# Optimization experiments

Measured on AMD Instinct MI355X. Metric: run time of the kernel, lower is better.

## Reference

```python
import jax, jax.numpy as jnp
import numpy as np
import math

B, N = 64, 16384
POS_IN, HID, DIR_IN = 63, 128, 27
COLOR_IN = HID + DIR_IN  # 155
POS_W, POS_B = POS_IN * HID, HID          # 8064, 128
SIG_W, SIG_B = HID * 1, 1                  # 128, 1
COL_W, COL_B = COLOR_IN * 3, 3             # 465... actually 155*3=465? no: 465
TOTAL = POS_W + POS_B + SIG_W + SIG_B + COL_W + COL_B  # 8717


def pos_encode(x, num_freqs):
    # x: [..., 3] -> [..., 3 + 2*3*num_freqs], order: x, (sin f0, cos f0, sin f1, cos f1, ...)
    freqs = (2.0 ** jnp.arange(num_freqs, dtype=x.dtype)) * math.pi  # [L]
    xb = x[..., None, :] * freqs[:, None]                            # [..., L, 3]
    sc = jnp.stack([jnp.sin(xb), jnp.cos(xb)], axis=-2)              # [..., L, 2, 3]
    sc = sc.reshape(*x.shape[:-1], num_freqs * 2 * x.shape[-1])
    return jnp.concatenate([x, sc], axis=-1)


def setup_inputs() -> dict:
    key = jax.random.key(0)
    k1, k2, k3 = jax.random.split(key, 3)
    positions = jax.random.normal(k1, (B, N, 3), dtype=jnp.float32)
    directions = jax.random.normal(k2, (B, N, 3), dtype=jnp.float32)
    params = jax.random.normal(k3, (B, TOTAL), dtype=jnp.float32) * 0.1
    return {"positions": positions, "directions": directions, "params": params}


def reference(positions, directions, params):
    pos_enc = pos_encode(positions, 10)   # [B, N, 63]
    dir_enc = pos_encode(directions, 4)   # [B, N, 27]

    i = 0
    pw = params[:, i:i + POS_W].reshape(B, HID, POS_IN); i += POS_W
    pb = params[:, i:i + POS_B]; i += POS_B
    sw = params[:, i:i + SIG_W].reshape(B, 1, HID); i += SIG_W
    sb = params[:, i:i + SIG_B]; i += SIG_B
    cw = params[:, i:i + COL_W].reshape(B, 3, COLOR_IN); i += COL_W
    cb = params[:, i:i + COL_B]

    h = jnp.einsum('bnd,bhd->bnh', pos_enc, pw) + pb[:, None, :]
    h = jax.nn.relu(h)                                   # [B, N, 128]
    sigma = jnp.einsum('bnh,boh->bno', h, sw) + sb[:, None, :]  # [B, N, 1]
    h_dir = jnp.concatenate([h, dir_enc], axis=-1)       # [B, N, 155]
    rgb = jnp.einsum('bnc,boc->bno', h_dir, cw) + cb[:, None, :]
    rgb = jax.nn.sigmoid(rgb)                            # [B, N, 3]
    return sigma, rgb
```

## Files before the change

kernel.cpp:

```cpp
#include <hip/hip_runtime.h>
#include <hip/hip_bf16.h>


#define NB 64
#define NRAY 16384
#define NTOTAL 8789
#define PI_F 3.14159265358979323846f

typedef short bf16x8 __attribute__((ext_vector_type(8)));
typedef float f32x16 __attribute__((ext_vector_type(16)));

union U8 { unsigned u[4]; bf16x8 v; };

__device__ __forceinline__ unsigned bfbits(float x) {
    __hip_bfloat16 h = __float2bfloat16(x);
    return (unsigned)*reinterpret_cast<unsigned short*>(&h);
}
__device__ __forceinline__ unsigned pk2(float a, float b) {
    return bfbits(a) | (bfbits(b) << 16);
}

__global__ __launch_bounds__(256, 2) void nerf_mfma_kernel(
    const float* __restrict__ pos,
    const float* __restrict__ dir,
    const float* __restrict__ params,
    float* __restrict__ out)
{
    const int tid  = threadIdx.x;
    const int lane = tid & 63;
    const int wid  = tid >> 6;
    const int hi   = lane >> 5;
    const int l31  = lane & 31;

    const int b     = blockIdx.x >> 4;
    const int chunk = (blockIdx.x & 15) << 10;
    const float* __restrict__ p = params + b * NTOTAL;

    __shared__ uint4 encs[2048];
    char* encb = reinterpret_cast<char*>(encs);

    bf16x8 aw[4][4];
    #pragma unroll
    for (int mt = 0; mt < 4; ++mt) {
        const int hrow = mt * 32 + l31;
        const float* wrow = p + hrow * 63;
        const float bias = p[8064 + hrow];
        #pragma unroll
        for (int ks = 0; ks < 4; ++ks) {
            U8 u;
            #pragma unroll
            for (int j = 0; j < 4; ++j) {
                const int k0 = ks * 16 + hi * 8 + 2 * j;
                const int k1 = k0 + 1;
                const float e0 = (k0 < 3) ? wrow[k0] : (k0 == 3 ? bias : wrow[k0 - 1]);
                const float e1 = (k1 < 3) ? wrow[k1] : (k1 == 3 ? bias : wrow[k1 - 1]);
                u.u[j] = pk2(e0, e1);
            }
            aw[mt][ks] = u.v;
        }
    }
    bf16x8 haw[8];
    {
        const int r = l31 & 3;
        const float* w2 = (r == 0) ? (p + 8192) : (p + 8321 + (r - 1) * 155);
        #pragma unroll
        for (int s = 0; s < 8; ++s) {
            const int base = 32 * (s >> 1) + 16 * (s & 1) + 4 * hi;
            U8 u;
            #pragma unroll
            for (int j = 0; j < 4; ++j) {
                const int i0 = 2 * j, i1 = 2 * j + 1;
                u.u[j] = pk2(w2[base + (i0 & 3) + 8 * (i0 >> 2)],
                             w2[base + (i1 & 3) + 8 * (i1 >> 2)]);
            }
            haw[s] = u.v;
        }
    }

    f32x16 FZ;
    #pragma unroll
    for (int i = 0; i < 16; ++i) FZ[i] = 0.f;

    const float sb  = p[8320];
    const float cb0 = p[8786], cb1 = p[8787], cb2 = p[8788];
    const float* __restrict__ cwr = p + 8321 + 128;
    const float* __restrict__ cwg = p + 8321 + 155 + 128;
    const float* __restrict__ cwb2 = p + 8321 + 310 + 128;

    const int rayBlock = b * NRAY + chunk;
    float* __restrict__ rgbout = out + (long)NB * NRAY;
    const long pbase = (long)(rayBlock + tid) * 3;

    float3 P  = *reinterpret_cast<const float3*>(pos + pbase);
    float3 Dv = *reinterpret_cast<const float3*>(dir + pbase);

    #pragma unroll 1
    for (int it = 0; it < 4; ++it) {
        const int ray = rayBlock + it * 256 + tid;

        float3 Pn, Dn;
        if (it < 3) {
            Pn = *reinterpret_cast<const float3*>(pos + pbase + (it + 1) * 768);
            Dn = *reinterpret_cast<const float3*>(dir + pbase + (it + 1) * 768);
        }

        {
            asm volatile("s_waitcnt lgkmcnt(0)" ::: "memory");
            const int swz = (tid & 7) << 4;
            char* myrow = encb + tid * 128;
            float s0, c0, s1, c1, s2, c2;
            __sincosf(P.x * PI_F, &s0, &c0);
            __sincosf(P.y * PI_F, &s1, &c1);
            __sincosf(P.z * PI_F, &s2, &c2);
            unsigned wb[4];
            wb[0] = pk2(P.x, P.y);
            wb[1] = pk2(P.z, 1.0f);
            #pragma unroll
            for (int f = 0; f < 10; ++f) {
                const int w = 2 + 3 * f;
                wb[(w + 0) & 3] = pk2(s0, s1);
                if (((w + 0) & 3) == 3) {
                    uint4 v; v.x = wb[0]; v.y = wb[1]; v.z = wb[2]; v.w = wb[3];
                    *reinterpret_cast<uint4*>(myrow + ((((w + 0) >> 2) * 16) ^ swz)) = v;
                }
                wb[(w + 1) & 3] = pk2(s2, c0);
                if (((w + 1) & 3) == 3) {
                    uint4 v; v.x = wb[0]; v.y = wb[1]; v.z = wb[2]; v.w = wb[3];
                    *reinterpret_cast<uint4*>(myrow + ((((w + 1) >> 2) * 16) ^ swz)) = v;
                }
                wb[(w + 2) & 3] = pk2(c1, c2);
                if (((w + 2) & 3) == 3) {
                    uint4 v; v.x = wb[0]; v.y = wb[1]; v.z = wb[2]; v.w = wb[3];
                    *reinterpret_cast<uint4*>(myrow + ((((w + 2) >> 2) * 16) ^ swz)) = v;
                }
                if (f < 9) {
                    float t;
                    t = 2.f * s0 * c0; c0 = fmaf(-2.f * s0, s0, 1.f); s0 = t;
                    t = 2.f * s1 * c1; c1 = fmaf(-2.f * s1, s1, 1.f); s1 = t;
                    t = 2.f * s2 * c2; c2 = fmaf(-2.f * s2, s2, 1.f); s2 = t;
                }
            }
            asm volatile("s_waitcnt lgkmcnt(0)" ::: "memory");
        }

        float hres[2][4];
        #pragma unroll
        for (int nt = 0; nt < 2; ++nt) {
            const int row = wid * 64 + nt * 32 + l31;
            const int swz = (row & 7) << 4;
            bf16x8 be[4];
            #pragma unroll
            for (int ks = 0; ks < 4; ++ks)
                be[ks] = *reinterpret_cast<const bf16x8*>(
                    encb + row * 128 + (((ks * 32 + hi * 16)) ^ swz));

            f32x16 haccA, haccB;
            #pragma unroll
            for (int mt = 0; mt < 4; ++mt) {
                f32x16 accm = __builtin_amdgcn_mfma_f32_32x32x16_bf16(aw[mt][0], be[0], FZ, 0, 0, 0);
                accm = __builtin_amdgcn_mfma_f32_32x32x16_bf16(aw[mt][1], be[1], accm, 0, 0, 0);
                accm = __builtin_amdgcn_mfma_f32_32x32x16_bf16(aw[mt][2], be[2], accm, 0, 0, 0);
                accm = __builtin_amdgcn_mfma_f32_32x32x16_bf16(aw[mt][3], be[3], accm, 0, 0, 0);

                #pragma unroll
                for (int t = 0; t < 2; ++t) {
                    const int rb = t * 8;
                    U8 u;
                    #pragma unroll
                    for (int j = 0; j < 4; ++j)
                        u.u[j] = pk2(fmaxf(accm[rb + 2 * j], 0.f),
                                     fmaxf(accm[rb + 2 * j + 1], 0.f));
                    const int s = 2 * mt + t;
                    if (t == 0)
                        haccA = __builtin_amdgcn_mfma_f32_32x32x16_bf16(
                            haw[s], u.v, (mt == 0) ? FZ : haccA, 0, 0, 0);
                    else
                        haccB = __builtin_amdgcn_mfma_f32_32x32x16_bf16(
                            haw[s], u.v, (mt == 0) ? FZ : haccB, 0, 0, 0);
                }
            }
            hres[nt][0] = haccA[0] + haccB[0];
            hres[nt][1] = haccA[1] + haccB[1];
            hres[nt][2] = haccA[2] + haccB[2];
            hres[nt][3] = haccA[3] + haccB[3];
        }

        const float hv0 = hi ? hres[1][0] : hres[0][0];
        const float hv1 = hi ? hres[1][1] : hres[0][1];
        const float hv2 = hi ? hres[1][2] : hres[0][2];
        const float hv3 = hi ? hres[1][3] : hres[0][3];

        float sig = hv0 + sb;
        float cr  = hv1 + cb0;
        float cg  = hv2 + cb1;
        float cbl = hv3 + cb2;

        {
            float s0, c0, s1, c1, s2, c2;
            __sincosf(Dv.x * PI_F, &s0, &c0);
            __sincosf(Dv.y * PI_F, &s1, &c1);
            __sincosf(Dv.z * PI_F, &s2, &c2);
            cr  = fmaf(Dv.x, cwr[0], cr);  cg  = fmaf(Dv.x, cwg[0], cg);  cbl = fmaf(Dv.x, cwb2[0], cbl);
            cr  = fmaf(Dv.y, cwr[1], cr);  cg  = fmaf(Dv.y, cwg[1], cg);  cbl = fmaf(Dv.y, cwb2[1], cbl);
            cr  = fmaf(Dv.z, cwr[2], cr);  cg  = fmaf(Dv.z, cwg[2], cg);  cbl = fmaf(Dv.z, cwb2[2], cbl);
            #pragma unroll
            for (int f = 0; f < 4; ++f) {
                const int j = 3 + 6 * f;
                cr = fmaf(s0, cwr[j+0], cr); cg = fmaf(s0, cwg[j+0], cg); cbl = fmaf(s0, cwb2[j+0], cbl);
                cr = fmaf(s1, cwr[j+1], cr); cg = fmaf(s1, cwg[j+1], cg); cbl = fmaf(s1, cwb2[j+1], cbl);
                cr = fmaf(s2, cwr[j+2], cr); cg = fmaf(s2, cwg[j+2], cg); cbl = fmaf(s2, cwb2[j+2], cbl);
                cr = fmaf(c0, cwr[j+3], cr); cg = fmaf(c0, cwg[j+3], cg); cbl = fmaf(c0, cwb2[j+3], cbl);
                cr = fmaf(c1, cwr[j+4], cr); cg = fmaf(c1, cwg[j+4], cg); cbl = fmaf(c1, cwb2[j+4], cbl);
                cr = fmaf(c2, cwr[j+5], cr); cg = fmaf(c2, cwg[j+5], cg); cbl = fmaf(c2, cwb2[j+5], cbl);
                if (f < 3) {
                    float t;
                    t = 2.f * s0 * c0; c0 = fmaf(-2.f * s0, s0, 1.f); s0 = t;
                    t = 2.f * s1 * c1; c1 = fmaf(-2.f * s1, s1, 1.f); s1 = t;
                    t = 2.f * s2 * c2; c2 = fmaf(-2.f * s2, s2, 1.f); s2 = t;
                }
            }
        }

        cr  = 1.0f / (1.0f + __expf(-cr));
        cg  = 1.0f / (1.0f + __expf(-cg));
        cbl = 1.0f / (1.0f + __expf(-cbl));

        out[ray] = sig;
        float3 rgbv; rgbv.x = cr; rgbv.y = cg; rgbv.z = cbl;
        *reinterpret_cast<float3*>(rgbout + (long)ray * 3) = rgbv;

        P = Pn; Dv = Dn;
    }
}

extern "C" void kernel_launch(void* const* d_in, const int* in_sizes, int n_in,
                              void* d_out, int out_size, void* d_ws, size_t ws_size,
                              hipStream_t stream) {
    const float* pos    = (const float*)d_in[0];
    const float* dirs   = (const float*)d_in[1];
    const float* params = (const float*)d_in[2];
    float* out = (float*)d_out;

    dim3 grid(1024);
    dim3 block(256);
    nerf_mfma_kernel<<<grid, block, 0, stream>>>(pos, dirs, params, out);
}
```

Before: 53.72 us.

## Software-pipeline positional encoding of next ray tile behind MFMA work

```diff
diff --git a/kernel.cpp b/kernel.cpp
--- a/kernel.cpp
+++ b/kernel.cpp
@@ -12,12 +12,10 @@
 
 union U8 { unsigned u[4]; bf16x8 v; };
 
-__device__ __forceinline__ unsigned bfbits(float x) {
-    __hip_bfloat16 h = __float2bfloat16(x);
-    return (unsigned)*reinterpret_cast<unsigned short*>(&h);
-}
 __device__ __forceinline__ unsigned pk2(float a, float b) {
-    return bfbits(a) | (bfbits(b) << 16);
+    float2 t; t.x = a; t.y = b;
+    __hip_bfloat162 h = __float22bfloat162_rn(t);
+    return *reinterpret_cast<unsigned*>(&h);
 }
 
 __global__ __launch_bounds__(256, 2) void nerf_mfma_kernel(
@@ -83,84 +81,82 @@
 
     const float sb  = p[8320];
     const float cb0 = p[8786], cb1 = p[8787], cb2 = p[8788];
-    const float* __restrict__ cwr = p + 8321 + 128;
-    const float* __restrict__ cwg = p + 8321 + 155 + 128;
+    const float* __restrict__ cwr  = p + 8321 + 128;
+    const float* __restrict__ cwg  = p + 8321 + 155 + 128;
     const float* __restrict__ cwb2 = p + 8321 + 310 + 128;
 
     const int rayBlock = b * NRAY + chunk;
     float* __restrict__ rgbout = out + (long)NB * NRAY;
-    const long pbase = (long)(rayBlock + tid) * 3;
-
-    float3 P  = *reinterpret_cast<const float3*>(pos + pbase);
-    float3 Dv = *reinterpret_cast<const float3*>(dir + pbase);
+    const long pb0 = (long)(rayBlock + tid) * 3;
+
+    auto encode_row = [&](const float3 Pv) {
+        const int swz = (tid & 7) << 4;
+        char* myrow = encb + tid * 128;
+        float s0, c0, s1, c1, s2, c2;
+        __sincosf(Pv.x * PI_F, &s0, &c0);
+        __sincosf(Pv.y * PI_F, &s1, &c1);
+        __sincosf(Pv.z * PI_F, &s2, &c2);
+        unsigned w[32];
+        w[0] = pk2(Pv.x, Pv.y);
+        w[1] = pk2(Pv.z, 1.0f);
+        #pragma unroll
+        for (int f = 0; f < 10; ++f) {
+            w[2 + 3 * f] = pk2(s0, s1);
+            w[3 + 3 * f] = pk2(s2, c0);
+            w[4 + 3 * f] = pk2(c1, c2);
+            if (f < 9) {
+                float t;
+                t = 2.f * s0 * c0; c0 = fmaf(-2.f * s0, s0, 1.f); s0 = t;
+                t = 2.f * s1 * c1; c1 = fmaf(-2.f * s1, s1, 1.f); s1 = t;
+                t = 2.f * s2 * c2; c2 = fmaf(-2.f * s2, s2, 1.f); s2 = t;
+            }
+        }
+        #pragma unroll
+        for (int cq = 0; cq < 8; ++cq) {
+            uint4 v;
+            v.x = w[4 * cq + 0]; v.y = w[4 * cq + 1];
+            v.z = w[4 * cq + 2]; v.w = w[4 * cq + 3];
+            *reinterpret_cast<uint4*>(myrow + ((cq * 16) ^ swz)) = v;
+        }
+    };
+
+    float3 P0 = *reinterpret_cast<const float3*>(pos + pb0);
+    float3 Pn = *reinterpret_cast<const float3*>(pos + pb0 + 768);
+    float3 Dc = *reinterpret_cast<const float3*>(dir + pb0);
+    encode_row(P0);
 
     #pragma unroll 1
     for (int it = 0; it < 4; ++it) {
         const int ray = rayBlock + it * 256 + tid;
 
-        float3 Pn, Dn;
-        if (it < 3) {
-            Pn = *reinterpret_cast<const float3*>(pos + pbase + (it + 1) * 768);
-            Dn = *reinterpret_cast<const float3*>(dir + pbase + (it + 1) * 768);
-        }
-
-        {
-            asm volatile("s_waitcnt lgkmcnt(0)" ::: "memory");
-            const int swz = (tid & 7) << 4;
-            char* myrow = encb + tid * 128;
-            float s0, c0, s1, c1, s2, c2;
-            __sincosf(P.x * PI_F, &s0, &c0);
-            __sincosf(P.y * PI_F, &s1, &c1);
-            __sincosf(P.z * PI_F, &s2, &c2);
-            unsigned wb[4];
-            wb[0] = pk2(P.x, P.y);
-            wb[1] = pk2(P.z, 1.0f);
-            #pragma unroll
-            for (int f = 0; f < 10; ++f) {
-                const int w = 2 + 3 * f;
-                wb[(w + 0) & 3] = pk2(s0, s1);
-                if (((w + 0) & 3) == 3) {
-                    uint4 v; v.x = wb[0]; v.y = wb[1]; v.z = wb[2]; v.w = wb[3];
-                    *reinterpret_cast<uint4*>(myrow + ((((w + 0) >> 2) * 16) ^ swz)) = v;
-                }
-                wb[(w + 1) & 3] = pk2(s2, c0);
-                if (((w + 1) & 3) == 3) {
-                    uint4 v; v.x = wb[0]; v.y = wb[1]; v.z = wb[2]; v.w = wb[3];
-                    *reinterpret_cast<uint4*>(myrow + ((((w + 1) >> 2) * 16) ^ swz)) = v;
-                }
-                wb[(w + 2) & 3] = pk2(c1, c2);
-                if (((w + 2) & 3) == 3) {
-                    uint4 v; v.x = wb[0]; v.y = wb[1]; v.z = wb[2]; v.w = wb[3];
-                    *reinterpret_cast<uint4*>(myrow + ((((w + 2) >> 2) * 16) ^ swz)) = v;
-                }
-                if (f < 9) {
-                    float t;
-                    t = 2.f * s0 * c0; c0 = fmaf(-2.f * s0, s0, 1.f); s0 = t;
-                    t = 2.f * s1 * c1; c1 = fmaf(-2.f * s1, s1, 1.f); s1 = t;
-                    t = 2.f * s2 * c2; c2 = fmaf(-2.f * s2, s2, 1.f); s2 = t;
-                }
-            }
-            asm volatile("s_waitcnt lgkmcnt(0)" ::: "memory");
-        }
-
-        float hres[2][4];
+        float3 Pn2, Dn;
+        if (it < 2) Pn2 = *reinterpret_cast<const float3*>(pos + pb0 + (it + 2) * 768);
+        if (it < 3) Dn  = *reinterpret_cast<const float3*>(dir + pb0 + (it + 1) * 768);
+
+        bf16x8 be[2][4];
         #pragma unroll
         for (int nt = 0; nt < 2; ++nt) {
             const int row = wid * 64 + nt * 32 + l31;
             const int swz = (row & 7) << 4;
-            bf16x8 be[4];
             #pragma unroll
             for (int ks = 0; ks < 4; ++ks)
-                be[ks] = *reinterpret_cast<const bf16x8*>(
-                    encb + row * 128 + (((ks * 32 + hi * 16)) ^ swz));
-
-            f32x16 haccA, haccB;
+                be[nt][ks] = *reinterpret_cast<const bf16x8*>(
+                    encb + row * 128 + ((ks * 32 + hi * 16) ^ swz));
+        }
+
+        if (it < 3) encode_row(Pn);
+
+        __builtin_amdgcn_s_setprio(1);
+        float hres[2][4];
+        #pragma unroll
+        for (int nt = 0; nt < 2; ++nt) {
+            f32x16 hacc;
             #pragma unroll
             for (int mt = 0; mt < 4; ++mt) {
-                f32x16 accm = __builtin_amdgcn_mfma_f32_32x32x16_bf16(aw[mt][0], be[0], FZ, 0, 0, 0);
-                accm = __builtin_amdgcn_mfma_f32_32x32x16_bf16(aw[mt][1], be[1], accm, 0, 0, 0);
-                accm = __builtin_amdgcn_mfma_f32_32x32x16_bf16(aw[mt][2], be[2], accm, 0, 0, 0);
-                accm = __builtin_amdgcn_mfma_f32_32x32x16_bf16(aw[mt][3], be[3], accm, 0, 0, 0);
+                f32x16 accm = __builtin_amdgcn_mfma_f32_32x32x16_bf16(aw[mt][0], be[nt][0], FZ, 0, 0, 0);
+                accm = __builtin_amdgcn_mfma_f32_32x32x16_bf16(aw[mt][1], be[nt][1], accm, 0, 0, 0);
+                accm = __builtin_amdgcn_mfma_f32_32x32x16_bf16(aw[mt][2], be[nt][2], accm, 0, 0, 0);
+                accm = __builtin_amdgcn_mfma_f32_32x32x16_bf16(aw[mt][3], be[nt][3], accm, 0, 0, 0);
 
                 #pragma unroll
                 for (int t = 0; t < 2; ++t) {
@@ -170,20 +166,14 @@
                     for (int j = 0; j < 4; ++j)
                         u.u[j] = pk2(fmaxf(accm[rb + 2 * j], 0.f),
                                      fmaxf(accm[rb + 2 * j + 1], 0.f));
-                    const int s = 2 * mt + t;
-                    if (t == 0)
-                        haccA = __builtin_amdgcn_mfma_f32_32x32x16_bf16(
-                            haw[s], u.v, (mt == 0) ? FZ : haccA, 0, 0, 0);
-                    else
-                        haccB = __builtin_amdgcn_mfma_f32_32x32x16_bf16(
-                            haw[s], u.v, (mt == 0) ? FZ : haccB, 0, 0, 0);
+                    hacc = __builtin_amdgcn_mfma_f32_32x32x16_bf16(
+                        haw[2 * mt + t], u.v, (mt == 0 && t == 0) ? FZ : hacc, 0, 0, 0);
                 }
             }
-            hres[nt][0] = haccA[0] + haccB[0];
-            hres[nt][1] = haccA[1] + haccB[1];
-            hres[nt][2] = haccA[2] + haccB[2];
-            hres[nt][3] = haccA[3] + haccB[3];
-        }
+            hres[nt][0] = hacc[0]; hres[nt][1] = hacc[1];
+            hres[nt][2] = hacc[2]; hres[nt][3] = hacc[3];
+        }
+        __builtin_amdgcn_s_setprio(0);
 
         const float hv0 = hi ? hres[1][0] : hres[0][0];
         const float hv1 = hi ? hres[1][1] : hres[0][1];
@@ -197,12 +187,12 @@
 
         {
             float s0, c0, s1, c1, s2, c2;
-            __sincosf(Dv.x * PI_F, &s0, &c0);
-            __sincosf(Dv.y * PI_F, &s1, &c1);
-            __sincosf(Dv.z * PI_F, &s2, &c2);
-            cr  = fmaf(Dv.x, cwr[0], cr);  cg  = fmaf(Dv.x, cwg[0], cg);  cbl = fmaf(Dv.x, cwb2[0], cbl);
-            cr  = fmaf(Dv.y, cwr[1], cr);  cg  = fmaf(Dv.y, cwg[1], cg);  cbl = fmaf(Dv.y, cwb2[1], cbl);
-            cr  = fmaf(Dv.z, cwr[2], cr);  cg  = fmaf(Dv.z, cwg[2], cg);  cbl = fmaf(Dv.z, cwb2[2], cbl);
+            __sincosf(Dc.x * PI_F, &s0, &c0);
+            __sincosf(Dc.y * PI_F, &s1, &c1);
+            __sincosf(Dc.z * PI_F, &s2, &c2);
+            cr  = fmaf(Dc.x, cwr[0], cr);  cg  = fmaf(Dc.x, cwg[0], cg);  cbl = fmaf(Dc.x, cwb2[0], cbl);
+            cr  = fmaf(Dc.y, cwr[1], cr);  cg  = fmaf(Dc.y, cwg[1], cg);  cbl = fmaf(Dc.y, cwb2[1], cbl);
+            cr  = fmaf(Dc.z, cwr[2], cr);  cg  = fmaf(Dc.z, cwg[2], cg);  cbl = fmaf(Dc.z, cwb2[2], cbl);
             #pragma unroll
             for (int f = 0; f < 4; ++f) {
                 const int j = 3 + 6 * f;
@@ -229,7 +219,7 @@
         float3 rgbv; rgbv.x = cr; rgbv.y = cg; rgbv.z = cbl;
         *reinterpret_cast<float3*>(rgbout + (long)ray * 3) = rgbv;
 
-        P = Pn; Dv = Dn;
+        Pn = Pn2; Dc = Dn;
     }
 }
 
```

Measured after the change: 53.83 us. Within noise of the previous version (+0.2%).
